# Kernel optimization log

Hardware: AMD Instinct MI355X
Metric: run time of the kernel (lower is better)

The kernel has to match this reference:

```python
import jax, jax.numpy as jnp
import numpy as np
import math

B, S, HID = 1, 2048, 2048
NH, NKV, HD = 32, 8, 64
GROUPS = NH // NKV
BOOST_SCALE, NARROW_SCALE = 1.0, 4.0
NEG = -1e9


def rope_cos_sin(seq_len, scale):
    inv_freq = 1.0 / (10000.0 ** (jnp.arange(0, HD, 2, dtype=jnp.float32) / HD))
    t = jnp.arange(seq_len, dtype=jnp.float32) / scale
    freqs = jnp.outer(t, inv_freq)                      # [s, hd/2]
    emb = jnp.concatenate([freqs, freqs], axis=-1)      # [s, hd]
    return jnp.cos(emb), jnp.sin(emb)


def rotate_half(x):
    x1, x2 = x[..., : HD // 2], x[..., HD // 2:]
    return jnp.concatenate([-x2, x1], axis=-1)


def apply_rope(q, k, cos, sin, position_ids):
    c = cos[position_ids][:, None]                      # [b,1,s,hd]
    s = sin[position_ids][:, None]
    return q * c + rotate_half(q) * s, k * c + rotate_half(k) * s


def setup_inputs() -> dict:
    key = jax.random.key(0)
    ks = jax.random.split(key, 5)
    hidden_states = jax.random.normal(ks[0], (B, S, HID), dtype=jnp.float32)
    i = jnp.arange(S)[:, None]
    j = jnp.arange(S)[None, :]
    attention_mask = jnp.where(j <= i, 0.0, NEG).astype(jnp.float32)[None, None]  # [1,1,S,S]
    position_ids = jnp.broadcast_to(jnp.arange(S, dtype=jnp.int32)[None], (B, S))
    sc = 1.0 / math.sqrt(HID)
    Wq = jax.random.normal(ks[1], (NH * HD, HID), dtype=jnp.float32) * sc
    Wk = jax.random.normal(ks[2], (NKV * HD, HID), dtype=jnp.float32) * sc
    Wv = jax.random.normal(ks[3], (NKV * HD, HID), dtype=jnp.float32) * sc
    Wo = jax.random.normal(ks[4], (HID, HID), dtype=jnp.float32) * sc
    return dict(hidden_states=hidden_states, attention_mask=attention_mask,
                position_ids=position_ids, Wq=Wq, Wk=Wk, Wv=Wv, Wo=Wo)


def reference(hidden_states, attention_mask, position_ids, Wq, Wk, Wv, Wo):
    b, q_len, _ = hidden_states.shape
    kv_seq_len = q_len

    q = (hidden_states @ Wq.T).reshape(b, q_len, NH, HD).transpose(0, 2, 1, 3)   # [b,H,s,hd]
    k = (hidden_states @ Wk.T).reshape(b, q_len, NKV, HD).transpose(0, 2, 1, 3)  # [b,Hkv,s,hd]
    v = (hidden_states @ Wv.T).reshape(b, q_len, NKV, HD).transpose(0, 2, 1, 3)

    boost_cos, boost_sin = rope_cos_sin(kv_seq_len, BOOST_SCALE)
    narrow_cos, narrow_sin = rope_cos_sin(kv_seq_len + 30, NARROW_SCALE)
    bq, bk = apply_rope(q, k, boost_cos, boost_sin, position_ids)
    nq, nk = apply_rope(q, k, narrow_cos, narrow_sin, position_ids)

    # repeat_kv (GQA)
    bk = jnp.repeat(bk, GROUPS, axis=1)
    nk = jnp.repeat(nk, GROUPS, axis=1)
    v = jnp.repeat(v, GROUPS, axis=1)

    inv_sqrt = 1.0 / math.sqrt(HD)
    big = jnp.einsum('bhqd,bhkd->bhqk', bq, bk) * inv_sqrt
    small = jnp.einsum('bhqd,bhkd->bhqk', nq, nk) * inv_sqrt
    big = big + attention_mask
    small = small + attention_mask

    # neighbor mask: tril minus (for rows >= context_length) tril(diag=context_length)
    # which zeroes those rows entirely -> neighbor = (j <= i) & (i < context_length)
    context_length = q_len - 10
    i = jnp.arange(q_len)[:, None]
    j = jnp.arange(kv_seq_len)[None, :]
    neighbor = (j <= i) & (i < context_length)

    merged = jnp.where(neighbor, big, small)
    probs = jax.nn.softmax(merged.astype(jnp.float32), axis=-1).astype(q.dtype)
    attn = jnp.einsum('bhqk,bhkd->bhqd', probs, v)
    attn = attn.transpose(0, 2, 1, 3).reshape(b, q_len, HID)
    return attn @ Wo.T
```

## Files before the change

kernel.cpp:

```cpp
#include <hip/hip_runtime.h>
#include <math.h>

#define S_LEN 2048
#define HIDN  2048
#define NH    32
#define NKV   8
#define HD    64
#define KVW   (NKV * HD)
#define CTX   (S_LEN - 10)

typedef unsigned short u16;
typedef __attribute__((ext_vector_type(4))) float f32x4;
typedef __attribute__((ext_vector_type(16))) float f32x16;
typedef __attribute__((ext_vector_type(8))) short s16x8;

#define QSCL 0.18033688011112042f
#define L2_1E4 13.287712379549449f

__device__ __forceinline__ float bf2f(u16 u) {
  union { unsigned int i; float f; } v; v.i = ((unsigned int)u) << 16; return v.f;
}
__device__ __forceinline__ u16 f2bf(float f) {
  union { float f; unsigned int i; } v; v.f = f;
  unsigned int r = v.i + 0x7fffu + ((v.i >> 16) & 1u);
  return (u16)(r >> 16);
}
__device__ __forceinline__ unsigned int cvt_pk_bf16(float a, float b) {
  unsigned int d;
  asm("v_cvt_pk_bf16_f32 %0, %1, %2" : "=v"(d) : "v"(a), "v"(b));
  return d;
}

__global__ __launch_bounds__(256) void conv_all(
    const float* __restrict__ h,  const float* __restrict__ wq,
    const float* __restrict__ wk, const float* __restrict__ wv,
    const float* __restrict__ wo,
    u16* __restrict__ Hb, u16* __restrict__ Wqb, u16* __restrict__ Wkb,
    u16* __restrict__ Wvb, u16* __restrict__ Wob)
{
  const int i = blockIdx.x * 256 + threadIdx.x;
  const float* src; u16* dst; int off;
  if      (i < 1048576) { src = h;  dst = Hb;  off = i; }
  else if (i < 2097152) { src = wq; dst = Wqb; off = i - 1048576; }
  else if (i < 2359296) { src = wk; dst = Wkb; off = i - 2097152; }
  else if (i < 2621440) { src = wv; dst = Wvb; off = i - 2359296; }
  else                  { src = wo; dst = Wob; off = i - 2621440; }
  const float4 f4 = ((const float4*)src)[off];
  ushort4 o4;
  o4.x = f2bf(f4.x); o4.y = f2bf(f4.y); o4.z = f2bf(f4.z); o4.w = f2bf(f4.w);
  ((ushort4*)dst)[off] = o4;
}

#define BM 128
#define BN 64
#define BK 64

template<int MODE>
__device__ __forceinline__ void gemm_body(
    u16* __restrict__ As, u16* __restrict__ Bs,
    const u16* __restrict__ A, const u16* __restrict__ B,
    void* __restrict__ Cv, void* __restrict__ Cv2,
    int N, int K, int row0, int col0, const int* __restrict__ pos)
{
  const int tid  = threadIdx.x;
  const int wave = tid >> 6;
  const int lane = tid & 63;
  const int l15  = lane & 15;
  const int wr   = wave * 32;

  f32x4 acc[2][4] = {};

  const int srow = wave * 8 + (lane >> 3);
  const int scol = (lane & 7) * 8;

  for (int kt = 0; kt < K; kt += BK) {
#pragma unroll
    for (int it = 0; it < 4; ++it) {
      const u16* gA = A + (size_t)(row0 + it * 32 + srow) * K + kt + scol;
      u16* lA = &As[(it * 32 + wave * 8) * BK];
      __builtin_amdgcn_global_load_lds((const __attribute__((address_space(1))) void*)gA,
                                       (__attribute__((address_space(3))) void*)lA, 16, 0, 0);
    }
#pragma unroll
    for (int it = 0; it < 2; ++it) {
      const u16* gB = B + (size_t)(col0 + it * 32 + srow) * K + kt + scol;
      u16* lB = &Bs[(it * 32 + wave * 8) * BK];
      __builtin_amdgcn_global_load_lds((const __attribute__((address_space(1))) void*)gB,
                                       (__attribute__((address_space(3))) void*)lB, 16, 0, 0);
    }
    __syncthreads();
#pragma unroll
    for (int kk = 0; kk < 2; ++kk) {
      const int ko = kk * 32 + (lane >> 4) * 8;
      s16x8 af[2], bg[4];
#pragma unroll
      for (int mi = 0; mi < 2; ++mi)
        af[mi] = *(const s16x8*)&As[(wr + mi * 16 + l15) * BK + ko];
#pragma unroll
      for (int ni = 0; ni < 4; ++ni)
        bg[ni] = *(const s16x8*)&Bs[(ni * 16 + l15) * BK + ko];
#pragma unroll
      for (int mi = 0; mi < 2; ++mi)
#pragma unroll
        for (int ni = 0; ni < 4; ++ni)
          acc[mi][ni] = __builtin_amdgcn_mfma_f32_16x16x32_bf16(af[mi], bg[ni], acc[mi][ni], 0, 0, 0);
    }
    __syncthreads();
  }

  const int rq = (lane >> 4) * 4;
  const int cq = l15;

  if (MODE == 3) {
#pragma unroll
    for (int mi = 0; mi < 2; ++mi)
#pragma unroll
      for (int ni = 0; ni < 4; ++ni) {
        const int r = row0 + wr + mi * 16 + rq;
        const int c = col0 + ni * 16 + cq;
#pragma unroll
        for (int t = 0; t < 4; ++t)
          ((float*)Cv)[(size_t)(r + t) * N + c] = acc[mi][ni][t];
      }
  } else if (MODE == 2) {
#pragma unroll
    for (int mi = 0; mi < 2; ++mi)
#pragma unroll
      for (int ni = 0; ni < 4; ++ni) {
        const int r = row0 + wr + mi * 16 + rq;
        const int c = col0 + ni * 16 + cq;
        ushort4 o4;
        o4.x = f2bf(acc[mi][ni][0]); o4.y = f2bf(acc[mi][ni][1]);
        o4.z = f2bf(acc[mi][ni][2]); o4.w = f2bf(acc[mi][ni][3]);
        *(ushort4*)&((u16*)Cv)[(size_t)c * S_LEN + r] = o4;
      }
  } else {
#pragma unroll
    for (int mi = 0; mi < 2; ++mi) {
#pragma unroll
      for (int t = 0; t < 4; ++t) {
        const int i = row0 + wr + mi * 16 + rq + t;
        const float fpos = (float)pos[i];
#pragma unroll
        for (int ni = 0; ni < 2; ++ni) {
          const int d = ni * 16 + cq;
          const int c = col0 + d;
          const float f = exp2f(-(float)(2 * d) * (1.0f / HD) * L2_1E4);
          const float x1 = acc[mi][ni][t], x2 = acc[mi][ni + 2][t];
          if (MODE == 0) {
            const float scl = (i < CTX) ? 1.0f : 0.25f;
            const float a  = fpos * scl * f;
            const float cs = __cosf(a), sn = __sinf(a);
            u16* Cq = (u16*)Cv;
            Cq[(size_t)i * N + c]      = f2bf((x1 * cs - x2 * sn) * QSCL);
            Cq[(size_t)i * N + c + 32] = f2bf((x2 * cs + x1 * sn) * QSCL);
          } else {
            const float ab = fpos * f, an = fpos * 0.25f * f;
            const float cb_ = __cosf(ab), sb_ = __sinf(ab);
            const float cn_ = __cosf(an), sn_ = __sinf(an);
            ((u16*)Cv)[(size_t)i * N + c]       = f2bf(x1 * cb_ - x2 * sb_);
            ((u16*)Cv)[(size_t)i * N + c + 32]  = f2bf(x2 * cb_ + x1 * sb_);
            ((u16*)Cv2)[(size_t)i * N + c]      = f2bf(x1 * cn_ - x2 * sn_);
            ((u16*)Cv2)[(size_t)i * N + c + 32] = f2bf(x2 * cn_ + x1 * sn_);
          }
        }
      }
    }
  }
}

__global__ __launch_bounds__(256) void gemm_qkv(
    const u16* __restrict__ A, const u16* __restrict__ Wq, const u16* __restrict__ Wk,
    const u16* __restrict__ Wv, u16* __restrict__ Q, u16* __restrict__ Kb,
    u16* __restrict__ Kn, u16* __restrict__ Vt, const int* __restrict__ pos)
{
  __shared__ u16 As[BM * BK];
  __shared__ u16 Bs[BN * BK];
  const int bn = blockIdx.x;
  const int row0 = blockIdx.y * BM;
  if (bn < 32)
    gemm_body<0>(As, Bs, A, Wq, Q, nullptr, HIDN, HIDN, row0, bn * BN, pos);
  else if (bn < 40)
    gemm_body<1>(As, Bs, A, Wk, Kb, Kn, KVW, HIDN, row0, (bn - 32) * BN, pos);
  else
    gemm_body<2>(As, Bs, A, Wv, Vt, nullptr, KVW, HIDN, row0, (bn - 40) * BN, pos);
}

__global__ __launch_bounds__(256) void gemm_out(
    const u16* __restrict__ A, const u16* __restrict__ B, float* __restrict__ C, int N, int K)
{
  __shared__ u16 As[BM * BK];
  __shared__ u16 Bs[BN * BK];
  gemm_body<3>(As, Bs, A, B, C, nullptr, N, K, blockIdx.y * BM, blockIdx.x * BN, 0);
}

#define PAD 8
__global__ __launch_bounds__(256) void attn_mfma(
    const u16* __restrict__ Q, const u16* __restrict__ K, const u16* __restrict__ Kn,
    const u16* __restrict__ Vt, u16* __restrict__ O)
{
  __shared__ __align__(16) u16 Ks[2][64][HD + PAD];
  __shared__ __align__(16) u16 Kns[2][64][HD + PAD];
  __shared__ __align__(16) u16 Vts[2][HD][64 + PAD];
  __shared__ __align__(16) float Of[64][64];
  __shared__ float Lf[2][32];
  __shared__ float Li[2][32];

  const int tid  = threadIdx.x;
  const int wave = tid >> 6;
  const int lane = tid & 63;
  const int l31  = lane & 31;
  const int hi   = lane >> 5;
  const int wr   = wave >> 1;
  const int wk   = wave & 1;
  const int h    = blockIdx.y;
  const int kh   = h >> 2;
  const int pr   = blockIdx.x;

  int sa[2], sb[2];
#pragma unroll
  for (int it = 0; it < 2; ++it) {
    const int u = it * 256 + tid;
    sa[it] = u >> 3;
    sb[it] = (u & 7) * 8;
  }

  for (int ph = 0; ph < 2; ++ph) {
    const int qt = ph ? pr : 31 - pr;
    const int i_base = qt * 64;
    const int rw0 = i_base + wr * 32;
    const bool mixed_blk = (qt == 31);
    const bool mixed_wv  = mixed_blk && (rw0 + 31 >= CTX);

    s16x8 bq[4];
#pragma unroll
    for (int i = 0; i < 4; ++i)
      bq[i] = *(const s16x8*)(Q + (size_t)(rw0 + l31) * HIDN + h * HD + i * 16 + hi * 8);

    f32x16 acc0 = {};
    f32x16 acc1 = {};
    float lsum = 0.f;

    const int ntiles = qt + 1;
    s16x8 kr[2], vr[2], knr[2];

    auto LOADT = [&](int tt) {
      const int jn = tt * 64;
#pragma unroll
      for (int it = 0; it < 2; ++it) {
        kr[it] = *(const s16x8*)(K  + (size_t)(jn + sa[it]) * KVW + kh * HD + sb[it]);
        vr[it] = *(const s16x8*)(Vt + (size_t)(kh * HD + sa[it]) * S_LEN + jn + sb[it]);
        if (mixed_blk) knr[it] = *(const s16x8*)(Kn + (size_t)(jn + sa[it]) * KVW + kh * HD + sb[it]);
      }
    };
    auto STORET = [&](int b) {
#pragma unroll
      for (int it = 0; it < 2; ++it) {
        *(s16x8*)&Ks[b][sa[it]][sb[it]]  = kr[it];
        *(s16x8*)&Vts[b][sa[it]][sb[it]] = vr[it];
        if (mixed_blk) *(s16x8*)&Kns[b][sa[it]][sb[it]] = knr[it];
      }
    };

    LOADT(0);
    STORET(0);
    if (ntiles > 1) LOADT(1);
    __syncthreads();

    for (int t = 0; t < ntiles; ++t) {
      const int cur = t & 1;
      if (t + 1 < ntiles) STORET(cur ^ 1);
      if (t + 2 < ntiles) LOADT(t + 2);

      const int jt = t * 64;
      const int j0 = jt + wk * 32;
      if (j0 <= rw0 + 31) {
        const bool needmask = (j0 + 31 > rw0);

        f32x16 sc = {};
#pragma unroll
        for (int i = 0; i < 4; ++i) {
          const s16x8 ak = *(const s16x8*)&Ks[cur][wk * 32 + l31][i * 16 + hi * 8];
          sc = __builtin_amdgcn_mfma_f32_32x32x16_bf16(ak, bq[i], sc, 0, 0, 0);
        }
        if (mixed_wv) {
          f32x16 scn = {};
#pragma unroll
          for (int i = 0; i < 4; ++i) {
            const s16x8 ak = *(const s16x8*)&Kns[cur][wk * 32 + l31][i * 16 + hi * 8];
            scn = __builtin_amdgcn_mfma_f32_32x32x16_bf16(ak, bq[i], scn, 0, 0, 0);
          }
          const bool nar = (rw0 + l31) >= CTX;
#pragma unroll
          for (int r = 0; r < 16; ++r) sc[r] = nar ? scn[r] : sc[r];
        }

        float p[16];
#pragma unroll
        for (int r = 0; r < 16; ++r) {
          float e = __builtin_amdgcn_exp2f(fminf(sc[r], 80.f));
          if (needmask) {
            const int key = j0 + (r & 3) + 8 * (r >> 2) + 4 * hi;
            e = (key > rw0 + l31) ? 0.f : e;
          }
          p[r] = e;
          lsum += e;
        }

        unsigned int c[4][2];
#pragma unroll
        for (int blk = 0; blk < 4; ++blk) {
          c[blk][0] = cvt_pk_bf16(p[4 * blk + 0], p[4 * blk + 1]);
          c[blk][1] = cvt_pk_bf16(p[4 * blk + 2], p[4 * blk + 3]);
        }

#pragma unroll
        for (int s = 0; s < 2; ++s) {
          unsigned int w0 = c[2 * s][0], w2 = c[2 * s + 1][0];
          unsigned int w1 = c[2 * s][1], w3 = c[2 * s + 1][1];
          asm("v_permlane32_swap_b32 %0, %1" : "+v"(w0), "+v"(w2));
          asm("v_permlane32_swap_b32 %0, %1" : "+v"(w1), "+v"(w3));
          union { unsigned int u[4]; s16x8 v; } af;
          af.u[0] = w0; af.u[1] = w1; af.u[2] = w2; af.u[3] = w3;
          const int kc = wk * 32 + s * 16 + hi * 8;
          const s16x8 v0 = *(const s16x8*)&Vts[cur][l31][kc];
          const s16x8 v1 = *(const s16x8*)&Vts[cur][32 + l31][kc];
          acc0 = __builtin_amdgcn_mfma_f32_32x32x16_bf16(af.v, v0, acc0, 0, 0, 0);
          acc1 = __builtin_amdgcn_mfma_f32_32x32x16_bf16(af.v, v1, acc1, 0, 0, 0);
        }
      }

      __syncthreads();
    }

    lsum += __shfl_xor(lsum, 32, 64);
    if (wk == 1) {
#pragma unroll
      for (int r = 0; r < 16; ++r) {
        const int rl = (r & 3) + 8 * (r >> 2) + 4 * hi;
        Of[wr * 32 + rl][l31]      = acc0[r];
        Of[wr * 32 + rl][l31 + 32] = acc1[r];
      }
      if (hi == 0) Lf[wr][l31] = lsum;
    }
    __syncthreads();
    if (wk == 0) {
      const float tot = lsum + Lf[wr][l31];
      const float inv = 1.0f / fmaxf(tot, 1e-30f);
      if (hi == 0) Li[wr][l31] = inv;
#pragma unroll
      for (int r = 0; r < 16; ++r) {
        const int rl = (r & 3) + 8 * (r >> 2) + 4 * hi;
        const float iv = Li[wr][rl];
        const size_t o = (size_t)(rw0 + rl) * HIDN + h * HD + l31;
        O[o]      = f2bf((acc0[r] + Of[wr * 32 + rl][l31])      * iv);
        O[o + 32] = f2bf((acc1[r] + Of[wr * 32 + rl][l31 + 32]) * iv);
      }
    }
    __syncthreads();
  }
}

extern "C" void kernel_launch(void* const* d_in, const int* in_sizes, int n_in,
                              void* d_out, int out_size, void* d_ws, size_t ws_size,
                              hipStream_t stream)
{
  const float* hidden = (const float*)d_in[0];
  const int* pos      = (const int*)d_in[2];
  const float* Wq = (const float*)d_in[3];
  const float* Wk = (const float*)d_in[4];
  const float* Wv = (const float*)d_in[5];
  const float* Wo = (const float*)d_in[6];
  float* out = (float*)d_out;

  char* ws = (char*)d_ws;
  u16* Qb  = (u16*)(ws);
  u16* Kbb = (u16*)(ws + (8u  << 20));
  u16* Knb = (u16*)(ws + (10u << 20));
  u16* Vtb = (u16*)(ws + (12u << 20));
  u16* Ab  = (u16*)(ws + (14u << 20));
  u16* Hb  = (u16*)(ws + (22u << 20));
  u16* Wqb = (u16*)(ws + (30u << 20));
  u16* Wkb = (u16*)(ws + (38u << 20));
  u16* Wvb = (u16*)(ws + (40u << 20));
  u16* Wob = (u16*)(ws + (42u << 20));

  conv_all<<<dim3(14336), 256, 0, stream>>>(hidden, Wq, Wk, Wv, Wo, Hb, Wqb, Wkb, Wvb, Wob);
  gemm_qkv<<<dim3(48, 16), 256, 0, stream>>>(Hb, Wqb, Wkb, Wvb, Qb, Kbb, Knb, Vtb, pos);
  attn_mfma<<<dim3(16, NH), 256, 0, stream>>>(Qb, Kbb, Knb, Vtb, Ab);
  gemm_out<<<dim3(32, 16), 256, 0, stream>>>(Ab, Wob, out, HIDN, HIDN);
}
```

Baseline: 252.1 us.

## Load attention K/V fragments directly from global into registers, drop LDS staging

The attention kernel no longer stages K, Kn and V^T tiles through double-buffered shared memory with block-wide barriers. Each wave now loads its own MFMA operand fragments straight from global memory into registers, ping-ponging two register sets, and computes a per-wave tile count so waves skip work independently. This removes the LDS round trip and the per-tile __syncthreads. In exchange, the two waves that share a query row pair each load the same K/V data, so global/L2 traffic and load latency exposure go up, and register pressure rises.

```diff
diff --git a/kernel.cpp b/kernel.cpp
--- a/kernel.cpp
+++ b/kernel.cpp
@@ -194,14 +194,10 @@
   gemm_body<3>(As, Bs, A, B, C, nullptr, N, K, blockIdx.y * BM, blockIdx.x * BN, 0);
 }
 
-#define PAD 8
 __global__ __launch_bounds__(256) void attn_mfma(
     const u16* __restrict__ Q, const u16* __restrict__ K, const u16* __restrict__ Kn,
     const u16* __restrict__ Vt, u16* __restrict__ O)
 {
-  __shared__ __align__(16) u16 Ks[2][64][HD + PAD];
-  __shared__ __align__(16) u16 Kns[2][64][HD + PAD];
-  __shared__ __align__(16) u16 Vts[2][HD][64 + PAD];
   __shared__ __align__(16) float Of[64][64];
   __shared__ float Lf[2][32];
   __shared__ float Li[2][32];
@@ -217,20 +213,15 @@
   const int kh   = h >> 2;
   const int pr   = blockIdx.x;
 
-  int sa[2], sb[2];
-#pragma unroll
-  for (int it = 0; it < 2; ++it) {
-    const int u = it * 256 + tid;
-    sa[it] = u >> 3;
-    sb[it] = (u & 7) * 8;
-  }
+  const u16* Kp  = K  + (size_t)(wk * 32 + l31) * KVW + kh * HD;
+  const u16* Knp = Kn + (size_t)(wk * 32 + l31) * KVW + kh * HD;
+  const u16* Vp  = Vt + (size_t)(kh * HD + l31) * S_LEN;
+  const u16* Vp2 = Vt + (size_t)(kh * HD + 32 + l31) * S_LEN;
 
   for (int ph = 0; ph < 2; ++ph) {
     const int qt = ph ? pr : 31 - pr;
-    const int i_base = qt * 64;
-    const int rw0 = i_base + wr * 32;
-    const bool mixed_blk = (qt == 31);
-    const bool mixed_wv  = mixed_blk && (rw0 + 31 >= CTX);
+    const int rw0 = qt * 64 + wr * 32;
+    const bool mixed_wv = (qt == 31) && (rw0 + 31 >= CTX);
 
     s16x8 bq[4];
 #pragma unroll
@@ -241,96 +232,86 @@
     f32x16 acc1 = {};
     float lsum = 0.f;
 
-    const int ntiles = qt + 1;
-    s16x8 kr[2], vr[2], knr[2];
-
-    auto LOADT = [&](int tt) {
-      const int jn = tt * 64;
-#pragma unroll
-      for (int it = 0; it < 2; ++it) {
-        kr[it] = *(const s16x8*)(K  + (size_t)(jn + sa[it]) * KVW + kh * HD + sb[it]);
-        vr[it] = *(const s16x8*)(Vt + (size_t)(kh * HD + sa[it]) * S_LEN + jn + sb[it]);
-        if (mixed_blk) knr[it] = *(const s16x8*)(Kn + (size_t)(jn + sa[it]) * KVW + kh * HD + sb[it]);
-      }
+    const int m    = rw0 + 31 - wk * 32;
+    const int nt_w = (m < 0) ? 0 : (m >> 6) + 1;
+
+    auto LK = [&](s16x8* d, int tt) {
+      const u16* p = Kp + (size_t)(tt * 64) * KVW;
+#pragma unroll
+      for (int i = 0; i < 4; ++i) d[i] = *(const s16x8*)(p + i * 16 + hi * 8);
     };
-    auto STORET = [&](int b) {
-#pragma unroll
-      for (int it = 0; it < 2; ++it) {
-        *(s16x8*)&Ks[b][sa[it]][sb[it]]  = kr[it];
-        *(s16x8*)&Vts[b][sa[it]][sb[it]] = vr[it];
-        if (mixed_blk) *(s16x8*)&Kns[b][sa[it]][sb[it]] = knr[it];
-      }
+    auto LV = [&](s16x8* d, int tt) {
+      const int c0 = tt * 64 + wk * 32 + hi * 8;
+      d[0] = *(const s16x8*)(Vp  + c0);
+      d[1] = *(const s16x8*)(Vp2 + c0);
+      d[2] = *(const s16x8*)(Vp  + c0 + 16);
+      d[3] = *(const s16x8*)(Vp2 + c0 + 16);
     };
 
-    LOADT(0);
-    STORET(0);
-    if (ntiles > 1) LOADT(1);
-    __syncthreads();
-
-    for (int t = 0; t < ntiles; ++t) {
-      const int cur = t & 1;
-      if (t + 1 < ntiles) STORET(cur ^ 1);
-      if (t + 2 < ntiles) LOADT(t + 2);
-
-      const int jt = t * 64;
-      const int j0 = jt + wk * 32;
-      if (j0 <= rw0 + 31) {
-        const bool needmask = (j0 + 31 > rw0);
-
-        f32x16 sc = {};
+    auto COMPUTE = [&](const s16x8* kf, const s16x8* vf, int t) {
+      const int j0 = t * 64 + wk * 32;
+      const bool needmask = (j0 + 31 > rw0);
+
+      f32x16 sc = {};
+#pragma unroll
+      for (int i = 0; i < 4; ++i)
+        sc = __builtin_amdgcn_mfma_f32_32x32x16_bf16(kf[i], bq[i], sc, 0, 0, 0);
+      if (mixed_wv) {
+        const u16* p = Knp + (size_t)(t * 64) * KVW;
+        f32x16 scn = {};
 #pragma unroll
         for (int i = 0; i < 4; ++i) {
-          const s16x8 ak = *(const s16x8*)&Ks[cur][wk * 32 + l31][i * 16 + hi * 8];
-          sc = __builtin_amdgcn_mfma_f32_32x32x16_bf16(ak, bq[i], sc, 0, 0, 0);
+          const s16x8 ak = *(const s16x8*)(p + i * 16 + hi * 8);
+          scn = __builtin_amdgcn_mfma_f32_32x32x16_bf16(ak, bq[i], scn, 0, 0, 0);
         }
-        if (mixed_wv) {
-          f32x16 scn = {};
-#pragma unroll
-          for (int i = 0; i < 4; ++i) {
-            const s16x8 ak = *(const s16x8*)&Kns[cur][wk * 32 + l31][i * 16 + hi * 8];
-            scn = __builtin_amdgcn_mfma_f32_32x32x16_bf16(ak, bq[i], scn, 0, 0, 0);
-          }
-          const bool nar = (rw0 + l31) >= CTX;
-#pragma unroll
-          for (int r = 0; r < 16; ++r) sc[r] = nar ? scn[r] : sc[r];
+        const bool nar = (rw0 + l31) >= CTX;
+#pragma unroll
+        for (int r = 0; r < 16; ++r) sc[r] = nar ? scn[r] : sc[r];
+      }
+
+      float p[16];
+#pragma unroll
+      for (int r = 0; r < 16; ++r) {
+        float e = __builtin_amdgcn_exp2f(fminf(sc[r], 80.f));
+        if (needmask) {
+          const int key = j0 + (r & 3) + 8 * (r >> 2) + 4 * hi;
+          e = (key > rw0 + l31) ? 0.f : e;
         }
-
-        float p[16];
-#pragma unroll
-        for (int r = 0; r < 16; ++r) {
-          float e = __builtin_amdgcn_exp2f(fminf(sc[r], 80.f));
-          if (needmask) {
-            const int key = j0 + (r & 3) + 8 * (r >> 2) + 4 * hi;
-            e = (key > rw0 + l31) ? 0.f : e;
-          }
-          p[r] = e;
-          lsum += e;
-        }
-
-        unsigned int c[4][2];
-#pragma unroll
-        for (int blk = 0; blk < 4; ++blk) {
-          c[blk][0] = cvt_pk_bf16(p[4 * blk + 0], p[4 * blk + 1]);
-          c[blk][1] = cvt_pk_bf16(p[4 * blk + 2], p[4 * blk + 3]);
-        }
-
-#pragma unroll
-        for (int s = 0; s < 2; ++s) {
-          unsigned int w0 = c[2 * s][0], w2 = c[2 * s + 1][0];
-          unsigned int w1 = c[2 * s][1], w3 = c[2 * s + 1][1];
-          asm("v_permlane32_swap_b32 %0, %1" : "+v"(w0), "+v"(w2));
-          asm("v_permlane32_swap_b32 %0, %1" : "+v"(w1), "+v"(w3));
-          union { unsigned int u[4]; s16x8 v; } af;
-          af.u[0] = w0; af.u[1] = w1; af.u[2] = w2; af.u[3] = w3;
-          const int kc = wk * 32 + s * 16 + hi * 8;
-          const s16x8 v0 = *(const s16x8*)&Vts[cur][l31][kc];
-          const s16x8 v1 = *(const s16x8*)&Vts[cur][32 + l31][kc];
-          acc0 = __builtin_amdgcn_mfma_f32_32x32x16_bf16(af.v, v0, acc0, 0, 0, 0);
-          acc1 = __builtin_amdgcn_mfma_f32_32x32x16_bf16(af.v, v1, acc1, 0, 0, 0);
-        }
-      }
-
-      __syncthreads();
+        p[r] = e;
+        lsum += e;
+      }
+
+      unsigned int c[4][2];
+#pragma unroll
+      for (int blk = 0; blk < 4; ++blk) {
+        c[blk][0] = cvt_pk_bf16(p[4 * blk + 0], p[4 * blk + 1]);
+        c[blk][1] = cvt_pk_bf16(p[4 * blk + 2], p[4 * blk + 3]);
+      }
+
+#pragma unroll
+      for (int s = 0; s < 2; ++s) {
+        unsigned int w0 = c[2 * s][0], w2 = c[2 * s + 1][0];
+        unsigned int w1 = c[2 * s][1], w3 = c[2 * s + 1][1];
+        asm("v_permlane32_swap_b32 %0, %1" : "+v"(w0), "+v"(w2));
+        asm("v_permlane32_swap_b32 %0, %1" : "+v"(w1), "+v"(w3));
+        union { unsigned int u[4]; s16x8 v; } af;
+        af.u[0] = w0; af.u[1] = w1; af.u[2] = w2; af.u[3] = w3;
+        acc0 = __builtin_amdgcn_mfma_f32_32x32x16_bf16(af.v, vf[2 * s],     acc0, 0, 0, 0);
+        acc1 = __builtin_amdgcn_mfma_f32_32x32x16_bf16(af.v, vf[2 * s + 1], acc1, 0, 0, 0);
+      }
+    };
+
+    s16x8 ka[4], va[4], kb[4], vb[4];
+    int t = 0;
+    if (nt_w > 0) {
+      LK(ka, 0); LV(va, 0);
+      for (; t + 1 < nt_w; t += 2) {
+        LK(kb, t + 1); LV(vb, t + 1);
+        COMPUTE(ka, va, t);
+        if (t + 2 < nt_w) { LK(ka, t + 2); LV(va, t + 2); }
+        COMPUTE(kb, vb, t + 1);
+      }
+      if (t < nt_w) COMPUTE(ka, va, t);
     }
 
     lsum += __shfl_xor(lsum, 32, 64);
```

New measurement: 303.6 us. 1.2x slower.
